# Optimization experiments

Measured on AMD Instinct MI355X. Metric: run time of the kernel, lower is better.

Reference implementation:

```python
import jax, jax.numpy as jnp
import numpy as np
from jax import lax

STRIDE0, WS, PS, K = 4, 9, 3, 10
LVLS = 4
_MEAN = jnp.array([0.485, 0.456, 0.406], jnp.float32).reshape(1, 1, 3, 1, 1)
_STD = jnp.array([0.229, 0.224, 0.225], jnp.float32).reshape(1, 1, 3, 1, 1)


def _conv7(x, w, b):
    y = lax.conv_general_dilated(x, w, (1, 1), ((3, 3), (3, 3)),
                                 dimension_numbers=('NCHW', 'OIHW', 'NCHW'))
    return y + b[None, :, None, None]


def _basic(x, l, Ws):
    w1, b1, w2, b2, w3, b3, w4, b4, w5, b5 = [W[l] for W in Ws]
    x = jax.nn.relu(_conv7(x, w1, b1))
    x = jax.nn.relu(_conv7(x, w2, b2))
    x = jax.nn.relu(_conv7(x, w3, b3))
    x = jax.nn.relu(_conv7(x, w4, b4))
    return _conv7(x, w5, b5)


def _pool2(x):
    N, C, H, W = x.shape
    return x.reshape(N, C, H // 2, 2, W // 2, 2).mean(axis=(3, 5))


def _bsample(img, y, x):
    # img [N,C,H,W]; y,x [N,Hq,Wq] absolute float coords; border-clamped bilinear
    N, C, H, W = img.shape
    y = jnp.clip(y, 0., H - 1.)
    x = jnp.clip(x, 0., W - 1.)
    y0 = jnp.floor(y)
    x0 = jnp.floor(x)
    wy = (y - y0)[:, None]
    wx = (x - x0)[:, None]
    y0i = y0.astype(jnp.int32)
    x0i = x0.astype(jnp.int32)
    y1i = jnp.minimum(y0i + 1, H - 1)
    x1i = jnp.minimum(x0i + 1, W - 1)
    imgf = img.reshape(N, C, H * W)

    def g(yi, xi):
        idx = (yi * W + xi).reshape(N, 1, -1)
        return jnp.take_along_axis(imgf, idx, 2).reshape(N, C, *y.shape[1:])

    return (g(y0i, x0i) * (1 - wy) * (1 - wx) + g(y0i, x1i) * (1 - wy) * wx
            + g(y1i, x0i) * wy * (1 - wx) + g(y1i, x1i) * wy * wx)


def _spynet(ref, supp, Ws):
    # coarse-to-fine residual flow estimation (SpyNet)
    refs, sups = [ref], [supp]
    for _ in range(LVLS - 1):
        refs.append(_pool2(refs[-1]))
        sups.append(_pool2(sups[-1]))
    N = ref.shape[0]
    Hc, Wc = refs[-1].shape[2:]
    flow = jnp.zeros((N, 2, Hc, Wc), ref.dtype)
    for l in range(LVLS - 1, -1, -1):
        Hl, Wl = refs[l].shape[2:]
        if l < LVLS - 1:
            flow = 2. * jax.image.resize(flow, (N, 2, Hl, Wl), 'bilinear')
        gy, gx = jnp.meshgrid(jnp.arange(Hl, dtype=flow.dtype),
                              jnp.arange(Wl, dtype=flow.dtype), indexing='ij')
        warped = _bsample(sups[l], gy[None] + flow[:, 1], gx[None] + flow[:, 0])
        flow = flow + _basic(jnp.concatenate([refs[l], warped, flow], 1), l, Ws)
    return flow


def _bgather(vidf, ry, rx, H, W, C):
    # vidf [B,T,C,H*W]; ry,rx [B,T,*rest] float coords pre-clipped to valid range
    B, T = vidf.shape[:2]
    rest = ry.shape[2:]
    y0 = jnp.floor(ry)
    x0 = jnp.floor(rx)
    wy = (ry - y0)[:, :, None]
    wx = (rx - x0)[:, :, None]
    y0i = y0.astype(jnp.int32)
    x0i = x0.astype(jnp.int32)
    y1i = jnp.minimum(y0i + 1, H - 1)
    x1i = jnp.minimum(x0i + 1, W - 1)

    def g(yi, xi):
        idx = (yi * W + xi).reshape(B, T, 1, -1)
        return jnp.take_along_axis(vidf, idx, 3).reshape(B, T, C, *rest)

    return (g(y0i, x0i) * (1 - wy) * (1 - wx) + g(y0i, x1i) * (1 - wy) * wx
            + g(y1i, x0i) * wy * (1 - wx) + g(y1i, x1i) * wy * wx)


def _forward(vid, Ws):
    B, T, C, H, W = vid.shape
    # --- SpyNet flows between consecutive frames ---
    nv = (vid - _MEAN) / _STD
    ref = nv[:, :-1].reshape(B * (T - 1), C, H, W)
    sup = nv[:, 1:].reshape(B * (T - 1), C, H, W)
    fflow = _spynet(ref, sup, Ws).reshape(B, T - 1, 2, H, W)
    bflow = _spynet(sup, ref, Ws).reshape(B, T - 1, 2, H, W)
    z = jnp.zeros((B, 1, 2, H, W), vid.dtype)
    fflow = jnp.concatenate([fflow, z], 1)  # flow t -> t+1 (last frame zero)
    bflow = jnp.concatenate([z, bflow], 1)  # flow t -> t-1 (first frame zero)

    # --- flow-guided windowed non-local search (wt=1, skip_self=False) ---
    nH, nW = H // STRIDE0, W // STRIDE0
    qh = jnp.arange(nH) * STRIDE0
    qw = jnp.arange(nW) * STRIDE0
    fg = fflow[:, :, :, qh][:, :, :, :, qw]  # [B,T,2,nH,nW] flow at query grid
    bg = bflow[:, :, :, qh][:, :, :, :, qw]
    dp = jnp.arange(PS) - PS // 2
    offs = jnp.arange(WS) - WS // 2
    oh = jnp.repeat(offs, WS).astype(vid.dtype)  # [WS*WS] row offsets
    ow = jnp.tile(offs, WS).astype(vid.dtype)    # [WS*WS] col offsets

    # query patches (integer grid, clamped)
    yqi = jnp.clip(qh[:, None] + dp[None], 0, H - 1)
    xqi = jnp.clip(qw[:, None] + dp[None], 0, W - 1)
    qp = vid[:, :, :, yqi][..., xqi]           # [B,T,C,nH,PS,nW,PS]
    qp = qp.transpose(0, 1, 2, 3, 5, 4, 6)     # [B,T,C,nH,nW,PS,PS]
    qpe = qp[:, :, :, :, :, None, None]        # broadcast over (ws,ws)

    vidf = vid.reshape(B, T, C, H * W)
    qhf = qh.astype(vid.dtype)
    qwf = qw.astype(vid.dtype)
    offsf = offs.astype(vid.dtype)
    dpf = dp.astype(vid.dtype)
    zf = jnp.zeros((B, T, nH, nW), vid.dtype)

    flows_k = []
    for dt, fh, fw in ((0, zf, zf), (1, fg[:, :, 1], fg[:, :, 0]),
                       (-1, bg[:, :, 1], bg[:, :, 0])):
        tid = jnp.clip(jnp.arange(T) + dt, 0, T - 1)
        frf = vidf[:, tid]  # target frames, edge-clamped in time
        ry = (qhf[None, None, :, None, None, None] + fh[:, :, :, :, None, None]
              + offsf[None, None, None, None, :, None]
              + dpf[None, None, None, None, None, :])  # [B,T,nH,nW,WS,PS]
        rx = (qwf[None, None, None, :, None, None] + fw[:, :, :, :, None, None]
              + offsf[None, None, None, None, :, None]
              + dpf[None, None, None, None, None, :])
        ry = jnp.clip(ry, 0., H - 1.)
        rx = jnp.clip(rx, 0., W - 1.)
        RY = jnp.broadcast_to(ry[:, :, :, :, :, None, :, None],
                              (B, T, nH, nW, WS, WS, PS, PS))
        RX = jnp.broadcast_to(rx[:, :, :, :, None, :, None, :],
                              (B, T, nH, nW, WS, WS, PS, PS))
        cand = _bgather(frf, RY, RX, H, W, C)  # [B,T,C,nH,nW,WS,WS,PS,PS]
        dist = ((qpe - cand) ** 2).sum(axis=(2, -2, -1))  # [B,T,nH,nW,WS,WS]
        dist = dist.reshape(B, T, nH, nW, WS * WS)
        _, idx = lax.top_k(-dist, K)  # [B,T,nH,nW,K]
        dh = fh[..., None] + oh[idx]
        dw = fw[..., None] + ow[idx]
        dts = jnp.full_like(dh, float(dt))
        flows_k.append(jnp.stack([dts, dh, dw], axis=-1))
    return jnp.concatenate(flows_k, axis=-2)  # [B,T,nH,nW,3*K,3]


def setup_inputs():
    key = jax.random.key(0)
    ks = jax.random.split(key, 6)
    B, T, C, H, W = 1, 4, 3, 192, 192
    L = LVLS

    def w(k, shape):
        return jax.random.normal(k, shape, jnp.float32) * 0.02

    return {
        "vid": jax.random.normal(ks[0], (B, T, C, H, W), jnp.float32),
        "w1": w(ks[1], (L, 32, 8, 7, 7)), "b1": jnp.zeros((L, 32), jnp.float32),
        "w2": w(ks[2], (L, 64, 32, 7, 7)), "b2": jnp.zeros((L, 64), jnp.float32),
        "w3": w(ks[3], (L, 32, 64, 7, 7)), "b3": jnp.zeros((L, 32), jnp.float32),
        "w4": w(ks[4], (L, 16, 32, 7, 7)), "b4": jnp.zeros((L, 16), jnp.float32),
        "w5": w(ks[5], (L, 2, 16, 7, 7)), "b5": jnp.zeros((L, 2), jnp.float32),
    }


def reference(vid, w1, b1, w2, b2, w3, b3, w4, b4, w5, b5):
    return _forward(vid, (w1, b1, w2, b2, w3, b3, w4, b4, w5, b5))
```

## Files before the change

kernel.cpp:

```cpp
#include <hip/hip_runtime.h>
#include <cstdint>

#define H0 192
#define W0 192
#define TT 4
#define NBATCH 6

__global__ void k_normalize(const float* __restrict__ vid, float* __restrict__ nv) {
    int idx = blockIdx.x * 256 + threadIdx.x;
    const int total = TT * 3 * H0 * W0;
    if (idx >= total) return;
    int c = (idx / (H0 * W0)) % 3;
    float m = (c == 0) ? 0.485f : (c == 1) ? 0.456f : 0.406f;
    float s = (c == 0) ? 0.229f : (c == 1) ? 0.224f : 0.225f;
    nv[idx] = (vid[idx] - m) / s;
}

__global__ void k_pool(const float* __restrict__ in, float* __restrict__ out,
                       int NC, int Ho, int Wo) {
    int idx = blockIdx.x * 256 + threadIdx.x;
    int total = NC * Ho * Wo;
    if (idx >= total) return;
    int x = idx % Wo;
    int y = (idx / Wo) % Ho;
    int nc = idx / (Wo * Ho);
    const float* p = in + ((size_t)nc * (Ho * 2) + y * 2) * (size_t)(Wo * 2) + x * 2;
    int Wi = Wo * 2;
    out[idx] = (p[0] + p[1] + p[Wi] + p[Wi + 1]) * 0.25f;
}

__global__ void k_upsample2x(const float* __restrict__ in, float* __restrict__ out,
                             int NC, int Hi, int Wi) {
    int Ho = Hi * 2, Wo = Wi * 2;
    int idx = blockIdx.x * 256 + threadIdx.x;
    int total = NC * Ho * Wo;
    if (idx >= total) return;
    int x = idx % Wo;
    int y = (idx / Wo) % Ho;
    int nc = idx / (Wo * Ho);
    int ky = y >> 1, kx = x >> 1;
    int y0, y1, x0, x1;
    float wy0, wy1, wx0, wx1;
    if ((y & 1) == 0) {
        if (ky == 0) { y0 = 0; y1 = 0; wy0 = 1.f; wy1 = 0.f; }
        else { y0 = ky - 1; y1 = ky; wy0 = 0.25f; wy1 = 0.75f; }
    } else {
        if (ky == Hi - 1) { y0 = ky; y1 = ky; wy0 = 1.f; wy1 = 0.f; }
        else { y0 = ky; y1 = ky + 1; wy0 = 0.75f; wy1 = 0.25f; }
    }
    if ((x & 1) == 0) {
        if (kx == 0) { x0 = 0; x1 = 0; wx0 = 1.f; wx1 = 0.f; }
        else { x0 = kx - 1; x1 = kx; wx0 = 0.25f; wx1 = 0.75f; }
    } else {
        if (kx == Wi - 1) { x0 = kx; x1 = kx; wx0 = 1.f; wx1 = 0.f; }
        else { x0 = kx; x1 = kx + 1; wx0 = 0.75f; wx1 = 0.25f; }
    }
    const float* base = in + (size_t)nc * Hi * Wi;
    float v = wy0 * (wx0 * base[(size_t)y0 * Wi + x0] + wx1 * base[(size_t)y0 * Wi + x1])
            + wy1 * (wx0 * base[(size_t)y1 * Wi + x0] + wx1 * base[(size_t)y1 * Wi + x1]);
    out[idx] = 2.0f * v;
}

__global__ void k_build_in8(const float* __restrict__ pyr, const float* __restrict__ flow,
                            float* __restrict__ in8, int H, int W) {
    int idx = blockIdx.x * 256 + threadIdx.x;
    int total = NBATCH * H * W;
    if (idx >= total) return;
    int x = idx % W;
    int y = (idx / W) % H;
    int n = idx / (W * H);
    int ref_f = (n < 3) ? n : n - 2;
    int sup_f = (n < 3) ? n + 1 : n - 3;
    size_t hw = (size_t)H * W;
    float fx = flow[((size_t)n * 2 + 0) * hw + (size_t)y * W + x];
    float fy = flow[((size_t)n * 2 + 1) * hw + (size_t)y * W + x];
    float ry = (float)y + fy;
    float rx = (float)x + fx;
    ry = fminf(fmaxf(ry, 0.f), (float)(H - 1));
    rx = fminf(fmaxf(rx, 0.f), (float)(W - 1));
    float y0f = floorf(ry), x0f = floorf(rx);
    float wy = ry - y0f, wx = rx - x0f;
    int y0 = (int)y0f, x0 = (int)x0f;
    int y1 = min(y0 + 1, H - 1), x1 = min(x0 + 1, W - 1);
    const float* sup = pyr + (size_t)sup_f * 3 * hw;
    const float* ref = pyr + (size_t)ref_f * 3 * hw;
    float* o = in8 + (size_t)n * 8 * hw + (size_t)y * W + x;
    #pragma unroll
    for (int c = 0; c < 3; c++) {
        const float* sc = sup + (size_t)c * hw;
        float g00 = sc[(size_t)y0 * W + x0], g01 = sc[(size_t)y0 * W + x1];
        float g10 = sc[(size_t)y1 * W + x0], g11 = sc[(size_t)y1 * W + x1];
        float v = g00 * (1.f - wy) * (1.f - wx) + g01 * (1.f - wy) * wx
                + g10 * wy * (1.f - wx) + g11 * wy * wx;
        o[(size_t)(3 + c) * hw] = v;
        o[(size_t)c * hw] = ref[(size_t)c * hw + (size_t)y * W + x];
    }
    o[6 * hw] = fx;
    o[7 * hw] = fy;
}


#define IW 38
#define ISTR 44
#define NI (IW * IW)
#define ISZ (IW * ISTR)
#define NR 6

__device__ __forceinline__ void conv_iload(const float* __restrict__ ip, float* sreg,
        int tid, int by, int bx, int H, int W) {
    #pragma unroll
    for (int k = 0; k < NR; k++) {
        int tpos = tid + k * 256;
        int ly = tpos / IW;
        int lx = tpos - ly * IW;
        int gy = by + ly - 3, gx = bx + lx - 3;
        bool ok = (tpos < NI) && ((unsigned)gy < (unsigned)H) && ((unsigned)gx < (unsigned)W);
        sreg[k] = ok ? ip[gy * W + gx] : 0.f;
    }
}

__device__ __forceinline__ void conv_istore(float* __restrict__ dst, const float* sreg,
        int tid) {
    #pragma unroll
    for (int k = 0; k < NR; k++) {
        int tpos = tid + k * 256;
        int ly = tpos / IW;
        int lx = tpos - ly * IW;
        if (tpos < NI) dst[ly * ISTR + lx] = sreg[k];
    }
}

template<int OCB, int NWR>
__device__ __forceinline__ void conv_wload(const float* __restrict__ wt, float* wreg,
        int tid, int oc0, int IC, int cbase) {
    constexpr int NWELEM = OCB * 4 * 49;
    #pragma unroll
    for (int k = 0; k < NWR; k++) {
        int tpos = tid + k * 256;
        int oc = tpos / 196;
        int rem = tpos - oc * 196;
        int icc = rem / 49;
        int kk = rem - icc * 49;
        wreg[k] = (tpos < NWELEM) ? wt[((size_t)(oc0 + oc) * IC + (cbase + icc)) * 49 + kk] : 0.f;
    }
}

template<int OCB, bool RELU, bool ACC>
__global__ __launch_bounds__(256) void k_conv(
        const float* __restrict__ in, const float* __restrict__ wt,
        const float* __restrict__ bias, float* __restrict__ out,
        int IC, int OC, int H, int W, int ntx, int nty, int nocg) {
    constexpr int NWELEM = OCB * 4 * 49;
    constexpr int NWR = (NWELEM + 255) / 256;
    __shared__ float smi[2 * ISZ];
    __shared__ float smw[4 * OCB * 7 * 8];

    int nwg = gridDim.x, wg = blockIdx.x;
    int q = nwg >> 3, r = nwg & 7;
    int xcd = wg & 7, pos = wg >> 3;
    int logical = ((xcd < r) ? xcd * (q + 1) : r * (q + 1) + (xcd - r) * q) + pos;
    int ocg = logical % nocg; int t2 = logical / nocg;
    int tx = t2 % ntx; t2 /= ntx;
    int ty = t2 % nty; int n = t2 / nty;
    int oc0 = ocg * OCB;
    int bx = tx * 32, by = ty * 32;
    int tid = threadIdx.x;
    int tq = tid & 7, trow = tid >> 3;
    int hw = H * W;

    float acc[OCB][4];
    #pragma unroll
    for (int o = 0; o < OCB; o++)
        #pragma unroll
        for (int p = 0; p < 4; p++) acc[o][p] = 0.f;

    const float* ip0 = in + (size_t)n * IC * hw;
    float sreg[NR];
    float wreg[NWR];

    conv_wload<OCB, NWR>(wt, wreg, tid, oc0, IC, 0);
    conv_iload(ip0, sreg, tid, by, bx, H, W);
    conv_istore(smi, sreg, tid);
    if (IC > 1) conv_iload(ip0 + hw, sreg, tid, by, bx, H, W);

    for (int ic = 0; ic < IC; ++ic) {
        int cur = ic & 1;
        if ((ic & 3) == 0) {
            #pragma unroll
            for (int k = 0; k < NWR; k++) {
                int tpos = tid + k * 256;
                if (tpos < NWELEM) {
                    int oc = tpos / 196;
                    int rem = tpos - oc * 196;
                    int icc = rem / 49;
                    int kk = rem - icc * 49;
                    int ky = kk / 7, kx = kk - ky * 7;
                    smw[((icc * OCB + oc) * 7 + ky) * 8 + kx] = wreg[k];
                }
            }
            __syncthreads();
            if (ic + 4 < IC) conv_wload<OCB, NWR>(wt, wreg, tid, oc0, IC, ic + 4);
        }
        if (ic + 1 < IC) {
            conv_istore(smi + (cur ^ 1) * ISZ, sreg, tid);
            if (ic + 2 < IC)
                conv_iload(ip0 + (size_t)(ic + 2) * hw, sreg, tid, by, bx, H, W);
        }
        int icc = ic & 3;
        const float* smc = smi + cur * ISZ + trow * ISTR + tq * 4;
        #pragma unroll
        for (int ky = 0; ky < 7; ++ky) {
            float4 xa = *(const float4*)(smc + ky * ISTR);
            float4 xb = *(const float4*)(smc + ky * ISTR + 4);
            float2 xc = *(const float2*)(smc + ky * ISTR + 8);
            float xin[10] = {xa.x, xa.y, xa.z, xa.w, xb.x, xb.y, xb.z, xb.w, xc.x, xc.y};
            #pragma unroll
            for (int oc = 0; oc < OCB; ++oc) {
                const float4* wp = (const float4*)(smw + ((icc * OCB + oc) * 7 + ky) * 8);
                float4 wa = wp[0], wb = wp[1];
                float wv[7] = {wa.x, wa.y, wa.z, wa.w, wb.x, wb.y, wb.z};
                #pragma unroll
                for (int kx = 0; kx < 7; ++kx) {
                    #pragma unroll
                    for (int p = 0; p < 4; p++)
                        acc[oc][p] = fmaf(xin[kx + p], wv[kx], acc[oc][p]);
                }
            }
        }
        __syncthreads();
    }

    int ox0 = bx + tq * 4;
    int oy = by + trow;
    if (oy < H) {
        #pragma unroll
        for (int oc = 0; oc < OCB; ++oc) {
            float bv = bias[oc0 + oc];
            float v[4];
            #pragma unroll
            for (int p = 0; p < 4; p++) {
                v[p] = acc[oc][p] + bv;
                if (RELU) v[p] = fmaxf(v[p], 0.f);
            }
            float* op = out + ((size_t)n * OC + oc0 + oc) * hw + (size_t)oy * W + ox0;
            if (ox0 + 3 < W) {
                if (ACC) {
                    float4 o4 = *(const float4*)op;
                    o4.x += v[0]; o4.y += v[1]; o4.z += v[2]; o4.w += v[3];
                    *(float4*)op = o4;
                } else {
                    *(float4*)op = make_float4(v[0], v[1], v[2], v[3]);
                }
            } else {
                #pragma unroll
                for (int p = 0; p < 4; p++)
                    if (ox0 + p < W) { if (ACC) op[p] += v[p]; else op[p] = v[p]; }
            }
        }
    }
}

__global__ __launch_bounds__(64) void k_match(
        const float* __restrict__ vid, const float* __restrict__ flow,
        float* __restrict__ out) {
    int q = blockIdx.x;
    int j = q % 48; q /= 48;
    int i = q % 48; q /= 48;
    int t = q % 4;
    int dtIdx = q / 4;
    int lane = threadIdx.x;

    float fh = 0.f, fw = 0.f, dtf = 0.f;
    int tid = t;
    if (dtIdx == 1) {
        if (t < 3) {
            size_t base = (((size_t)t * 2) * 192 + i * 4) * 192 + j * 4;
            fw = flow[base];
            fh = flow[base + (size_t)192 * 192];
        }
        tid = min(t + 1, 3);
        dtf = 1.f;
    } else if (dtIdx == 2) {
        if (t > 0) {
            size_t base = (((size_t)(t + 2) * 2) * 192 + i * 4) * 192 + j * 4;
            fw = flow[base];
            fh = flow[base + (size_t)192 * 192];
        }
        tid = max(t - 1, 0);
        dtf = -1.f;
    }

    __shared__ int sy0[27], sy1[27], sx0[27], sx1[27];
    __shared__ float sfy[27], sfx[27], qp[27];
    if (lane < 27) {
        int wq = lane / 3, p = lane % 3;
        float ry = (((float)(i * 4) + fh) + (float)(wq - 4)) + (float)(p - 1);
        ry = fminf(fmaxf(ry, 0.f), 191.f);
        float y0f = floorf(ry);
        int y0 = (int)y0f;
        sy0[lane] = y0; sy1[lane] = min(y0 + 1, 191); sfy[lane] = ry - y0f;
        float rx = (((float)(j * 4) + fw) + (float)(wq - 4)) + (float)(p - 1);
        rx = fminf(fmaxf(rx, 0.f), 191.f);
        float x0f = floorf(rx);
        int x0 = (int)x0f;
        sx0[lane] = x0; sx1[lane] = min(x0 + 1, 191); sfx[lane] = rx - x0f;
        int c = lane / 9, pp = lane % 9, py = pp / 3, px = pp % 3;
        int yy = min(max(i * 4 + py - 1, 0), 191);
        int xx = min(max(j * 4 + px - 1, 0), 191);
        qp[lane] = vid[(((size_t)t * 3 + c) * 192 + yy) * 192 + xx];
    }
    __syncthreads();

    const float* frame = vid + (size_t)tid * 3 * 192 * 192;
    float dist[2];
    int widx[2];
    #pragma unroll
    for (int r = 0; r < 2; r++) {
        int w = lane + 64 * r;
        if (w < 81) {
            int wy = w / 9, wx = w % 9;
            float dsum = 0.f;
            for (int c = 0; c < 3; c++) {
                const float* fc = frame + (size_t)c * 36864;
                #pragma unroll
                for (int py = 0; py < 3; py++) {
                    int ye = wy * 3 + py;
                    int y0 = sy0[ye], y1 = sy1[ye];
                    float fy = sfy[ye];
                    const float* r0 = fc + (size_t)y0 * 192;
                    const float* r1 = fc + (size_t)y1 * 192;
                    #pragma unroll
                    for (int px = 0; px < 3; px++) {
                        int xe = wx * 3 + px;
                        int x0 = sx0[xe], x1 = sx1[xe];
                        float fx = sfx[xe];
                        float g00 = r0[x0], g01 = r0[x1], g10 = r1[x0], g11 = r1[x1];
                        float cand = g00 * (1.f - fy) * (1.f - fx) + g01 * (1.f - fy) * fx
                                   + g10 * fy * (1.f - fx) + g11 * fy * fx;
                        float diff = qp[(c * 3 + py) * 3 + px] - cand;
                        dsum = fmaf(diff, diff, dsum);
                    }
                }
            }
            dist[r] = dsum; widx[r] = w;
        } else {
            dist[r] = __builtin_inff(); widx[r] = 1000;
        }
    }

    for (int k = 0; k < 10; k++) {
        float d = dist[0]; int wi = widx[0];
        if (dist[1] < d || (dist[1] == d && widx[1] < wi)) { d = dist[1]; wi = widx[1]; }
        #pragma unroll
        for (int off = 32; off >= 1; off >>= 1) {
            float od = __shfl_xor(d, off);
            int ow = __shfl_xor(wi, off);
            if (od < d || (od == d && ow < wi)) { d = od; wi = ow; }
        }
        if (lane == 0) {
            size_t ob = ((((size_t)t * 48 + i) * 48 + j) * 30 + dtIdx * 10 + k) * 3;
            out[ob + 0] = dtf;
            out[ob + 1] = fh + (float)(wi / 9 - 4);
            out[ob + 2] = fw + (float)(wi % 9 - 4);
        }
        if (widx[0] == wi) dist[0] = __builtin_inff();
        if (widx[1] == wi) dist[1] = __builtin_inff();
    }
}

extern "C" void kernel_launch(void* const* d_in, const int* in_sizes, int n_in,
                              void* d_out, int out_size, void* d_ws, size_t ws_size,
                              hipStream_t stream) {
    const float* vid = (const float*)d_in[0];
    const float* w1 = (const float*)d_in[1];  const float* b1 = (const float*)d_in[2];
    const float* w2 = (const float*)d_in[3];  const float* b2 = (const float*)d_in[4];
    const float* w3 = (const float*)d_in[5];  const float* b3 = (const float*)d_in[6];
    const float* w4 = (const float*)d_in[7];  const float* b4 = (const float*)d_in[8];
    const float* w5 = (const float*)d_in[9];  const float* b5 = (const float*)d_in[10];
    float* out = (float*)d_out;
    float* ws = (float*)d_ws;

    float* nv    = ws;
    float* pyr1  = nv    + 442368;
    float* pyr2  = pyr1  + 110592;
    float* pyr3  = pyr2  + 27648;
    float* flowA = pyr3  + 6912;
    float* flowB = flowA + 442368;
    float* in8   = flowB + 442368;
    float* bufA  = in8   + 1769472;
    float* bufB  = bufA  + 7077888;

    k_normalize<<<(442368 + 255) / 256, 256, 0, stream>>>(vid, nv);
    k_pool<<<(110592 + 255) / 256, 256, 0, stream>>>(nv, pyr1, 12, 96, 96);
    k_pool<<<(27648 + 255) / 256, 256, 0, stream>>>(pyr1, pyr2, 12, 48, 48);
    k_pool<<<(6912 + 255) / 256, 256, 0, stream>>>(pyr2, pyr3, 12, 24, 24);

    const float* pyrs[4] = {nv, pyr1, pyr2, pyr3};

    float* cur = flowA;
    float* oth = flowB;
    hipMemsetAsync(cur, 0, (size_t)NBATCH * 2 * 24 * 24 * 4, stream);
    for (int l = 3; l >= 0; --l) {
        int H = H0 >> l, W = W0 >> l;
        if (l < 3) {
            k_upsample2x<<<((12 * H * W) + 255) / 256, 256, 0, stream>>>(cur, oth, 12, H / 2, W / 2);
            float* tsw = cur; cur = oth; oth = tsw;
        }
        k_build_in8<<<((NBATCH * H * W) + 255) / 256, 256, 0, stream>>>(pyrs[l], cur, in8, H, W);

        const float* W1 = w1 + (size_t)l * 32 * 8 * 49;  const float* B1 = b1 + l * 32;
        const float* W2 = w2 + (size_t)l * 64 * 32 * 49; const float* B2 = b2 + l * 64;
        const float* W3 = w3 + (size_t)l * 32 * 64 * 49; const float* B3 = b3 + l * 32;
        const float* W4 = w4 + (size_t)l * 16 * 32 * 49; const float* B4 = b4 + l * 16;
        const float* W5 = w5 + (size_t)l * 2 * 16 * 49;  const float* B5 = b5 + l * 2;

        int nt = (H + 31) / 32;
        int ntt = nt * nt;
        k_conv<4, true,  false><<<ntt * 8 * 6, 256, 0, stream>>>(in8,  W1, B1, bufA, 8,  32, H, W, nt, nt, 8);
        k_conv<8, true,  false><<<ntt * 8 * 6, 256, 0, stream>>>(bufA, W2, B2, bufB, 32, 64, H, W, nt, nt, 8);
        k_conv<8, true,  false><<<ntt * 4 * 6, 256, 0, stream>>>(bufB, W3, B3, bufA, 64, 32, H, W, nt, nt, 4);
        k_conv<4, true,  false><<<ntt * 4 * 6, 256, 0, stream>>>(bufA, W4, B4, bufB, 32, 16, H, W, nt, nt, 4);
        k_conv<2, false, true ><<<ntt * 1 * 6, 256, 0, stream>>>(bufB, W5, B5, cur,  16, 2,  H, W, nt, nt, 1);
    }

    k_match<<<27648, 64, 0, stream>>>(vid, cur, out);
}
```

Before: 3.329 ms.

## Load conv weights directly from global into registers with row prefetch

Drops the shared-memory weight staging in the 7x7 conv kernel. Each thread now reads weight rows straight from global memory, which are uniform across the block and should hit scalar or L1 cache, and it software-prefetches the next kernel row into registers. This removes the LDS weight traffic and the periodic staging stores. The output-channel block for conv2 and conv3 shrinks from 8 to 4, which doubles their grids and should reduce register pressure. The cost is more global load instructions in the inner loop, and each input tile is reused across fewer output channels.

Measured after the change: 3.261 ms. 2.0% less time.

```diff
diff --git a/kernel.cpp b/kernel.cpp
--- a/kernel.cpp
+++ b/kernel.cpp
@@ -130,30 +130,12 @@
     }
 }
 
-template<int OCB, int NWR>
-__device__ __forceinline__ void conv_wload(const float* __restrict__ wt, float* wreg,
-        int tid, int oc0, int IC, int cbase) {
-    constexpr int NWELEM = OCB * 4 * 49;
-    #pragma unroll
-    for (int k = 0; k < NWR; k++) {
-        int tpos = tid + k * 256;
-        int oc = tpos / 196;
-        int rem = tpos - oc * 196;
-        int icc = rem / 49;
-        int kk = rem - icc * 49;
-        wreg[k] = (tpos < NWELEM) ? wt[((size_t)(oc0 + oc) * IC + (cbase + icc)) * 49 + kk] : 0.f;
-    }
-}
-
 template<int OCB, bool RELU, bool ACC>
 __global__ __launch_bounds__(256) void k_conv(
         const float* __restrict__ in, const float* __restrict__ wt,
         const float* __restrict__ bias, float* __restrict__ out,
         int IC, int OC, int H, int W, int ntx, int nty, int nocg) {
-    constexpr int NWELEM = OCB * 4 * 49;
-    constexpr int NWR = (NWELEM + 255) / 256;
     __shared__ float smi[2 * ISZ];
-    __shared__ float smw[4 * OCB * 7 * 8];
 
     int nwg = gridDim.x, wg = blockIdx.x;
     int q = nwg >> 3, r = nwg & 7;
@@ -176,56 +158,57 @@
 
     const float* ip0 = in + (size_t)n * IC * hw;
     float sreg[NR];
-    float wreg[NWR];
-
-    conv_wload<OCB, NWR>(wt, wreg, tid, oc0, IC, 0);
+
     conv_iload(ip0, sreg, tid, by, bx, H, W);
     conv_istore(smi, sreg, tid);
     if (IC > 1) conv_iload(ip0 + hw, sreg, tid, by, bx, H, W);
 
+    float wl[OCB][7];
+    #pragma unroll
+    for (int oc = 0; oc < OCB; ++oc) {
+        const float* wp = wt + ((size_t)(oc0 + oc) * IC) * 49;
+        #pragma unroll
+        for (int kk = 0; kk < 7; ++kk) wl[oc][kk] = wp[kk];
+    }
+    __syncthreads();
+
     for (int ic = 0; ic < IC; ++ic) {
         int cur = ic & 1;
-        if ((ic & 3) == 0) {
-            #pragma unroll
-            for (int k = 0; k < NWR; k++) {
-                int tpos = tid + k * 256;
-                if (tpos < NWELEM) {
-                    int oc = tpos / 196;
-                    int rem = tpos - oc * 196;
-                    int icc = rem / 49;
-                    int kk = rem - icc * 49;
-                    int ky = kk / 7, kx = kk - ky * 7;
-                    smw[((icc * OCB + oc) * 7 + ky) * 8 + kx] = wreg[k];
-                }
-            }
-            __syncthreads();
-            if (ic + 4 < IC) conv_wload<OCB, NWR>(wt, wreg, tid, oc0, IC, ic + 4);
-        }
         if (ic + 1 < IC) {
             conv_istore(smi + (cur ^ 1) * ISZ, sreg, tid);
             if (ic + 2 < IC)
                 conv_iload(ip0 + (size_t)(ic + 2) * hw, sreg, tid, by, bx, H, W);
         }
-        int icc = ic & 3;
         const float* smc = smi + cur * ISZ + trow * ISTR + tq * 4;
         #pragma unroll
         for (int ky = 0; ky < 7; ++ky) {
+            float wn[OCB][7];
+            int nic = (ky == 6) ? ((ic + 1 < IC) ? ic + 1 : ic) : ic;
+            int nky = (ky == 6) ? 0 : ky + 1;
+            #pragma unroll
+            for (int oc = 0; oc < OCB; ++oc) {
+                const float* wp = wt + ((size_t)(oc0 + oc) * IC + nic) * 49 + nky * 7;
+                #pragma unroll
+                for (int kk = 0; kk < 7; ++kk) wn[oc][kk] = wp[kk];
+            }
             float4 xa = *(const float4*)(smc + ky * ISTR);
             float4 xb = *(const float4*)(smc + ky * ISTR + 4);
             float2 xc = *(const float2*)(smc + ky * ISTR + 8);
             float xin[10] = {xa.x, xa.y, xa.z, xa.w, xb.x, xb.y, xb.z, xb.w, xc.x, xc.y};
             #pragma unroll
             for (int oc = 0; oc < OCB; ++oc) {
-                const float4* wp = (const float4*)(smw + ((icc * OCB + oc) * 7 + ky) * 8);
-                float4 wa = wp[0], wb = wp[1];
-                float wv[7] = {wa.x, wa.y, wa.z, wa.w, wb.x, wb.y, wb.z};
                 #pragma unroll
                 for (int kx = 0; kx < 7; ++kx) {
+                    float wv = wl[oc][kx];
                     #pragma unroll
                     for (int p = 0; p < 4; p++)
-                        acc[oc][p] = fmaf(xin[kx + p], wv[kx], acc[oc][p]);
+                        acc[oc][p] = fmaf(xin[kx + p], wv, acc[oc][p]);
                 }
             }
+            #pragma unroll
+            for (int oc = 0; oc < OCB; ++oc)
+                #pragma unroll
+                for (int kk = 0; kk < 7; ++kk) wl[oc][kk] = wn[oc][kk];
         }
         __syncthreads();
     }
@@ -416,11 +399,11 @@
 
         int nt = (H + 31) / 32;
         int ntt = nt * nt;
-        k_conv<4, true,  false><<<ntt * 8 * 6, 256, 0, stream>>>(in8,  W1, B1, bufA, 8,  32, H, W, nt, nt, 8);
-        k_conv<8, true,  false><<<ntt * 8 * 6, 256, 0, stream>>>(bufA, W2, B2, bufB, 32, 64, H, W, nt, nt, 8);
-        k_conv<8, true,  false><<<ntt * 4 * 6, 256, 0, stream>>>(bufB, W3, B3, bufA, 64, 32, H, W, nt, nt, 4);
-        k_conv<4, true,  false><<<ntt * 4 * 6, 256, 0, stream>>>(bufA, W4, B4, bufB, 32, 16, H, W, nt, nt, 4);
-        k_conv<2, false, true ><<<ntt * 1 * 6, 256, 0, stream>>>(bufB, W5, B5, cur,  16, 2,  H, W, nt, nt, 1);
+        k_conv<4, true,  false><<<ntt * 8 * 6,  256, 0, stream>>>(in8,  W1, B1, bufA, 8,  32, H, W, nt, nt, 8);
+        k_conv<4, true,  false><<<ntt * 16 * 6, 256, 0, stream>>>(bufA, W2, B2, bufB, 32, 64, H, W, nt, nt, 16);
+        k_conv<4, true,  false><<<ntt * 8 * 6,  256, 0, stream>>>(bufB, W3, B3, bufA, 64, 32, H, W, nt, nt, 8);
+        k_conv<4, true,  false><<<ntt * 4 * 6,  256, 0, stream>>>(bufA, W4, B4, bufB, 32, 16, H, W, nt, nt, 4);
+        k_conv<2, false, true ><<<ntt * 1 * 6,  256, 0, stream>>>(bufB, W5, B5, cur,  16, 2,  H, W, nt, nt, 1);
     }
 
     k_match<<<27648, 64, 0, stream>>>(vid, cur, out);
```
